# Kernel optimization log

Measured on AMD Instinct MI355X. Metric: run time of the kernel, lower is better.

Reference implementation:

```python
import jax, jax.numpy as jnp
import numpy as np

N_NODES = 100000


def gcn_conv(x, edge_index, W, b, n_nodes):
    """PyG GCNConv: add self-loops, symmetric deg norm, linear, scatter-add, bias."""
    self_loops = jnp.arange(n_nodes, dtype=edge_index.dtype)
    src = jnp.concatenate([edge_index[0], self_loops])  # [E+N]
    dst = jnp.concatenate([edge_index[1], self_loops])  # [E+N]
    xw = x @ W  # [N, out]
    deg = jax.ops.segment_sum(jnp.ones_like(dst, dtype=xw.dtype), dst, num_segments=n_nodes)
    deg_inv_sqrt = jnp.where(deg > 0, jax.lax.rsqrt(deg), 0.0)
    norm = deg_inv_sqrt[src] * deg_inv_sqrt[dst]  # [E+N]
    msg = xw[src] * norm[:, None]                 # [E+N, out]
    out = jax.ops.segment_sum(msg, dst, num_segments=n_nodes)
    return out + b


def setup_inputs() -> dict:
    key = jax.random.key(0)
    ks = jax.random.split(key, 8)
    n, e, d_in, h = N_NODES, 3200000, 128, 16
    x = jax.random.normal(ks[0], (n, d_in), dtype=jnp.float32)
    edge_index = jax.random.randint(ks[1], (2, e), 0, n, dtype=jnp.int64)
    W1 = jax.random.normal(ks[2], (d_in, h), dtype=jnp.float32) / np.sqrt(d_in)
    b1 = jnp.zeros((h,), dtype=jnp.float32)
    W2 = jax.random.normal(ks[3], (h, h), dtype=jnp.float32) / np.sqrt(h)
    b2 = jnp.zeros((h,), dtype=jnp.float32)
    W_lin = jax.random.normal(ks[4], (h, 1), dtype=jnp.float32) / np.sqrt(h)
    b_lin = jnp.zeros((1,), dtype=jnp.float32)
    return {"x": x, "edge_index": edge_index, "W1": W1, "b1": b1,
            "W2": W2, "b2": b2, "W_lin": W_lin, "b_lin": b_lin}


def reference(x, edge_index, W1, b1, W2, b2, W_lin, b_lin):
    n = x.shape[0]
    h = gcn_conv(x, edge_index, W1, b1, n)
    h = jax.nn.relu(h)
    # dropout is identity in eval mode (training=False)
    h = gcn_conv(h, edge_index, W2, b2, n)
    h = jax.nn.relu(h)
    out = h @ W_lin + b_lin  # [N, 1]
    return out.squeeze(-1)   # [N]
```

## Files before the change

kernel.cpp:

```cpp
#include <hip/hip_runtime.h>
#include <hip/hip_fp16.h>

#define DIN 128
#define HDIM 16
#define NB 512
#define BDIV_MAX 256
#define CAPB 7168
#define HSTR 17
#define BIN_EPT 16
#define BINSZ (256 * BIN_EPT)
#define FXS 65536.0f
#define FXI (1.0f / 65536.0f)

__device__ __forceinline__ float4 f4add(float4 a, float4 b) {
    return make_float4(a.x + b.x, a.y + b.y, a.z + b.z, a.w + b.w);
}

__device__ __forceinline__ float4 h4_to_f4(uint2 u) {
    __half2 a = *(__half2*)&u.x, b = *(__half2*)&u.y;
    float2 fa = __half22float2(a), fb = __half22float2(b);
    return make_float4(fa.x, fa.y, fb.x, fb.y);
}
__device__ __forceinline__ uint2 f4_to_h4(float4 v) {
    __half2 a = __floats2half2_rn(v.x, v.y);
    __half2 b = __floats2half2_rn(v.z, v.w);
    uint2 u;
    u.x = *(unsigned*)&a;
    u.y = *(unsigned*)&b;
    return u;
}

__device__ __forceinline__ int load_idx(const void* ei, long long i, int is64) {
    return is64 ? (int)((const long long*)ei)[i] : ((const int*)ei)[i];
}

__device__ __forceinline__ void fx_acc(int* a, float4 v) {
    atomicAdd(a + 0, __float2int_rn(v.x * FXS));
    atomicAdd(a + 1, __float2int_rn(v.y * FXS));
    atomicAdd(a + 2, __float2int_rn(v.z * FXS));
    atomicAdd(a + 3, __float2int_rn(v.w * FXS));
}

__global__ __launch_bounds__(256) void k_main(const void* __restrict__ ei, long long E,
                                              int bdiv, unsigned Mdiv,
                                              int* __restrict__ bcur,
                                              unsigned int* __restrict__ recs,
                                              const float* __restrict__ x,
                                              const float* __restrict__ W1,
                                              unsigned int* __restrict__ y1,
                                              int n, int nbin) {
    __shared__ int cnt[NB];
    __shared__ int base[NB];
    __shared__ float Ws[DIN * HDIM];
    int tid = threadIdx.x;
    if ((int)blockIdx.x < nbin) {
        unsigned probe = ((const unsigned*)ei)[1 + 2 * (tid & 63)];
        int is64 = (__ballot(probe != 0) == 0ull) ? 1 : 0;
        cnt[tid] = 0; cnt[tid + 256] = 0;
        __syncthreads();
        long long e0 = (long long)blockIdx.x * BINSZ;
        int s[BIN_EPT], dl[BIN_EPT], b[BIN_EPT];
        if (e0 + BINSZ <= E) {
            int d[BIN_EPT];
            if (is64) {
                const longlong2* ps = (const longlong2*)((const long long*)ei + e0);
                const longlong2* pd = (const longlong2*)((const long long*)ei + E + e0);
#pragma unroll
                for (int i = 0; i < BIN_EPT / 2; i++) {
                    longlong2 vs = ps[i * 256 + tid];
                    longlong2 vd = pd[i * 256 + tid];
                    s[2 * i + 0] = (int)vs.x; s[2 * i + 1] = (int)vs.y;
                    d[2 * i + 0] = (int)vd.x; d[2 * i + 1] = (int)vd.y;
                }
            } else {
                const int4* ps = (const int4*)((const int*)ei + e0);
                const int4* pd = (const int4*)((const int*)ei + E + e0);
#pragma unroll
                for (int i = 0; i < BIN_EPT / 4; i++) {
                    int4 vs = ps[i * 256 + tid];
                    int4 vd = pd[i * 256 + tid];
                    s[4 * i + 0] = vs.x; s[4 * i + 1] = vs.y;
                    s[4 * i + 2] = vs.z; s[4 * i + 3] = vs.w;
                    d[4 * i + 0] = vd.x; d[4 * i + 1] = vd.y;
                    d[4 * i + 2] = vd.z; d[4 * i + 3] = vd.w;
                }
            }
#pragma unroll
            for (int i = 0; i < BIN_EPT; i++) {
                int bb = Mdiv ? (int)__umulhi((unsigned)d[i], Mdiv) : d[i];
                b[i] = bb;
                dl[i] = d[i] - bb * bdiv;
                atomicAdd(&cnt[bb], 1);
            }
        } else {
#pragma unroll
            for (int i = 0; i < BIN_EPT; i++) {
                long long e = e0 + (long long)i * 256 + tid;
                if (e < E) {
                    s[i] = load_idx(ei, e, is64);
                    int d = load_idx(ei, E + e, is64);
                    int bb = Mdiv ? (int)__umulhi((unsigned)d, Mdiv) : d;
                    b[i] = bb;
                    dl[i] = d - bb * bdiv;
                    atomicAdd(&cnt[bb], 1);
                } else {
                    b[i] = -1;
                }
            }
        }
        __syncthreads();
        {
            int t = tid;
            base[t] = atomicAdd(&bcur[t], cnt[t]); cnt[t] = 0;
            t = tid + 256;
            base[t] = atomicAdd(&bcur[t], cnt[t]); cnt[t] = 0;
        }
        __syncthreads();
#pragma unroll
        for (int i = 0; i < BIN_EPT; i++) {
            if (b[i] >= 0) {
                int off = atomicAdd(&cnt[b[i]], 1);
                int pos = base[b[i]] + off;
                if (pos < CAPB) {
                    recs[(size_t)b[i] * CAPB + pos] =
                        ((unsigned)dl[i] << 18) | (unsigned)s[i];
                }
            }
        }
    } else {
        for (int i = tid; i < DIN * HDIM; i += 256) Ws[i] = W1[i];
        __syncthreads();
        int node = ((int)blockIdx.x - nbin) * 256 + tid;
        if (node >= n) return;
        uint2* yr = (uint2*)(y1 + (size_t)node * 8);
        float acc[HDIM];
#pragma unroll
        for (int f = 0; f < HDIM; f++) acc[f] = 0.f;
        const float4* xr = (const float4*)(x + (size_t)node * DIN);
#pragma unroll 8
        for (int k4 = 0; k4 < DIN / 4; k4++) {
            float4 xv = xr[k4];
            int k = k4 * 4;
#pragma unroll
            for (int f = 0; f < HDIM; f++) {
                acc[f] += xv.x * Ws[(k + 0) * HDIM + f];
                acc[f] += xv.y * Ws[(k + 1) * HDIM + f];
                acc[f] += xv.z * Ws[(k + 2) * HDIM + f];
                acc[f] += xv.w * Ws[(k + 3) * HDIM + f];
            }
        }
#pragma unroll
        for (int q = 0; q < 4; q++)
            yr[q] = f4_to_h4(make_float4(acc[q * 4 + 0], acc[q * 4 + 1],
                                         acc[q * 4 + 2], acc[q * 4 + 3]));
    }
}

__global__ __launch_bounds__(512) void k_deg(const unsigned int* __restrict__ recs,
                                             const int* __restrict__ bcur,
                                             float* __restrict__ dis,
                                             unsigned int* __restrict__ y1,
                                             int n, int bdiv) {
    __shared__ int cnt[BDIV_MAX];
    int tid = threadIdx.x, b = blockIdx.x;
    if (tid < BDIV_MAX) cnt[tid] = 0;
    __syncthreads();
    int lo = b * bdiv; if (lo > n) lo = n;
    int hi = lo + bdiv; if (hi > n) hi = n;
    int nd = hi - lo;
    int m = bcur[b]; if (m > CAPB) m = CAPB;
    const unsigned int* r = recs + (size_t)b * CAPB;
    for (int i = tid; i < m; i += 512)
        atomicAdd(&cnt[r[i] >> 18], 1);
    __syncthreads();
    int q = tid & 3, g = tid >> 2;
    uint2* yv = (uint2*)y1;
    for (int j = g; j < nd; j += 128) {
        int node = lo + j;
        float dv = rsqrtf((float)cnt[j] + 1.0f);
        if (q == 0) dis[node] = dv;
        float4 t = h4_to_f4(yv[(size_t)node * 4 + q]);
        yv[(size_t)node * 4 + q] =
            f4_to_h4(make_float4(t.x * dv, t.y * dv, t.z * dv, t.w * dv));
    }
}

__global__ __launch_bounds__(512) void k_agg1(const unsigned int* __restrict__ recs,
                                              const int* __restrict__ bcur,
                                              const float* __restrict__ dis,
                                              const unsigned int* __restrict__ y1,
                                              const float* __restrict__ b1,
                                              const float* __restrict__ W2,
                                              unsigned int* __restrict__ y2,
                                              int n, int bdiv) {
    __shared__ int acc[BDIV_MAX * HSTR];
    __shared__ float4 Ws4[HDIM][4];
    int tid = threadIdx.x, b = blockIdx.x;
    if (tid < HDIM * 4)
        ((float4*)Ws4)[tid] = ((const float4*)W2)[tid];
    int lo = b * bdiv; if (lo > n) lo = n;
    int hi = lo + bdiv; if (hi > n) hi = n;
    int nd = hi - lo;
    for (int i = tid; i < bdiv * HSTR; i += 512) acc[i] = 0;
    __syncthreads();
    int m = bcur[b]; if (m > CAPB) m = CAPB;
    const unsigned int* r = recs + (size_t)b * CAPB;
    const uint2* yv = (const uint2*)y1;
    int q = tid & 3, g = tid >> 2;
    int i = g;
    for (; i + 128 < m; i += 256) {
        unsigned r0 = r[i], r1 = r[i + 128];
        float4 v0 = h4_to_f4(yv[(size_t)(r0 & 0x3FFFFu) * 4 + q]);
        float4 v1 = h4_to_f4(yv[(size_t)(r1 & 0x3FFFFu) * 4 + q]);
        fx_acc(&acc[(r0 >> 18) * HSTR + q * 4], v0);
        fx_acc(&acc[(r1 >> 18) * HSTR + q * 4], v1);
    }
    if (i < m) {
        unsigned r0 = r[i];
        float4 v0 = h4_to_f4(yv[(size_t)(r0 & 0x3FFFFu) * 4 + q]);
        fx_acc(&acc[(r0 >> 18) * HSTR + q * 4], v0);
    }
    __syncthreads();
    float4 bb = ((const float4*)b1)[q];
    for (int j = g; j < nd; j += 128) {
        int node = lo + j;
        float dv = dis[node];
        int* ap = &acc[j * HSTR + q * 4];
        float4 a = make_float4((float)ap[0] * FXI, (float)ap[1] * FXI,
                               (float)ap[2] * FXI, (float)ap[3] * FXI);
        a = f4add(a, h4_to_f4(yv[(size_t)node * 4 + q]));
        float4 h;
        h.x = fmaxf(dv * a.x + bb.x, 0.f);
        h.y = fmaxf(dv * a.y + bb.y, 0.f);
        h.z = fmaxf(dv * a.z + bb.z, 0.f);
        h.w = fmaxf(dv * a.w + bb.w, 0.f);
        float4 o = make_float4(0.f, 0.f, 0.f, 0.f);
#pragma unroll
        for (int k = 0; k < 4; k++) {
            float4 hk;
            hk.x = __shfl(h.x, k, 4); hk.y = __shfl(h.y, k, 4);
            hk.z = __shfl(h.z, k, 4); hk.w = __shfl(h.w, k, 4);
            float hv[4] = {hk.x, hk.y, hk.z, hk.w};
#pragma unroll
            for (int c = 0; c < 4; c++) {
                float4 w = Ws4[k * 4 + c][q];
                o.x += hv[c] * w.x; o.y += hv[c] * w.y;
                o.z += hv[c] * w.z; o.w += hv[c] * w.w;
            }
        }
        ((uint2*)y2)[(size_t)node * 4 + q] =
            f4_to_h4(make_float4(o.x * dv, o.y * dv, o.z * dv, o.w * dv));
    }
}

__global__ __launch_bounds__(512) void k_agg2(const unsigned int* __restrict__ recs,
                                              const int* __restrict__ bcur,
                                              const float* __restrict__ dis,
                                              const unsigned int* __restrict__ y2,
                                              const float* __restrict__ b2,
                                              const float* __restrict__ Wlin,
                                              const float* __restrict__ blin,
                                              float* __restrict__ out,
                                              int n, int bdiv) {
    __shared__ int acc[BDIV_MAX * HSTR];
    int tid = threadIdx.x, b = blockIdx.x;
    int lo = b * bdiv; if (lo > n) lo = n;
    int hi = lo + bdiv; if (hi > n) hi = n;
    int nd = hi - lo;
    for (int i = tid; i < bdiv * HSTR; i += 512) acc[i] = 0;
    __syncthreads();
    int m = bcur[b]; if (m > CAPB) m = CAPB;
    const unsigned int* r = recs + (size_t)b * CAPB;
    const uint2* yv = (const uint2*)y2;
    int q = tid & 3, g = tid >> 2;
    int i = g;
    for (; i + 128 < m; i += 256) {
        unsigned r0 = r[i], r1 = r[i + 128];
        float4 v0 = h4_to_f4(yv[(size_t)(r0 & 0x3FFFFu) * 4 + q]);
        float4 v1 = h4_to_f4(yv[(size_t)(r1 & 0x3FFFFu) * 4 + q]);
        fx_acc(&acc[(r0 >> 18) * HSTR + q * 4], v0);
        fx_acc(&acc[(r1 >> 18) * HSTR + q * 4], v1);
    }
    if (i < m) {
        unsigned r0 = r[i];
        float4 v0 = h4_to_f4(yv[(size_t)(r0 & 0x3FFFFu) * 4 + q]);
        fx_acc(&acc[(r0 >> 18) * HSTR + q * 4], v0);
    }
    __syncthreads();
    float4 bb = ((const float4*)b2)[q];
    float4 wl = ((const float4*)Wlin)[q];
    for (int j = g; j < nd; j += 128) {
        int node = lo + j;
        float dv = dis[node];
        int* ap = &acc[j * HSTR + q * 4];
        float4 a = make_float4((float)ap[0] * FXI, (float)ap[1] * FXI,
                               (float)ap[2] * FXI, (float)ap[3] * FXI);
        a = f4add(a, h4_to_f4(yv[(size_t)node * 4 + q]));
        float v = 0.f;
        v += fmaxf(dv * a.x + bb.x, 0.f) * wl.x;
        v += fmaxf(dv * a.y + bb.y, 0.f) * wl.y;
        v += fmaxf(dv * a.z + bb.z, 0.f) * wl.z;
        v += fmaxf(dv * a.w + bb.w, 0.f) * wl.w;
        v += __shfl_xor(v, 1, 4);
        v += __shfl_xor(v, 2, 4);
        if (q == 0) out[node] = v + blin[0];
    }
}

extern "C" void kernel_launch(void* const* d_in, const int* in_sizes, int n_in,
                              void* d_out, int out_size, void* d_ws, size_t ws_size,
                              hipStream_t stream) {
    const float* x    = (const float*)d_in[0];
    const void*  ei   = d_in[1];
    const float* W1   = (const float*)d_in[2];
    const float* b1   = (const float*)d_in[3];
    const float* W2   = (const float*)d_in[4];
    const float* b2   = (const float*)d_in[5];
    const float* Wlin = (const float*)d_in[6];
    const float* blin = (const float*)d_in[7];
    float* out = (float*)d_out;

    const int n = in_sizes[0] / DIN;
    const long long E = in_sizes[1] / 2;
    const int bdiv = (n + NB - 1) / NB;
    const unsigned Mdiv = (bdiv > 1)
        ? (unsigned)(((1ull << 32) + (unsigned)bdiv - 1) / (unsigned)bdiv) : 0u;

    char* ws = (char*)d_ws;
    size_t off = 0;
    auto alloc = [&](size_t bytes) { char* p = ws + off; off += (bytes + 255) & ~(size_t)255; return p; };
    int*   bcur = (int*)alloc(NB * 4);
    float* dis  = (float*)alloc((size_t)n * 4);
    unsigned int* y1 = (unsigned int*)alloc((size_t)n * 8 * 4);
    unsigned int* y2 = (unsigned int*)alloc((size_t)n * 8 * 4);
    unsigned int* recs = (unsigned int*)alloc((size_t)NB * CAPB * 4);

    const int nb_xw  = (n + 255) / 256;
    const int nb_bin = (int)((E + BINSZ - 1) / BINSZ);

    hipMemsetAsync(bcur, 0, NB * sizeof(int), stream);
    k_main<<<nb_bin + nb_xw, 256, 0, stream>>>(ei, E, bdiv, Mdiv, bcur, recs, x, W1, y1, n, nb_bin);
    k_deg<<<NB, 512, 0, stream>>>(recs, bcur, dis, y1, n, bdiv);
    k_agg1<<<NB, 512, 0, stream>>>(recs, bcur, dis, y1, b1, W2, y2, n, bdiv);
    k_agg2<<<NB, 512, 0, stream>>>(recs, bcur, dis, y2, b2, Wlin, blin, out, n, bdiv);
}
```

Measured before the change: 203.4 us.

## Count degrees with global atomics during binning and stage records in LDS

The binning kernel now runs 512 threads per block and counts in-degrees directly with global atomics on a zeroed per-node array. This replaces the separate degree kernel, which re-read all the binned records, with a simple per-node normalisation kernel. The aggregation kernels copy each bucket's records into shared memory with vector loads and unroll the gather loop four-way to get more loads in flight. The cost is 3.2M scattered global atomics on the degree array and about 28KB of extra LDS per aggregation block, which can lower occupancy.

Result: slower. 294.5 us (+44.8%).

```diff
diff --git a/kernel.cpp b/kernel.cpp
--- a/kernel.cpp
+++ b/kernel.cpp
@@ -8,7 +8,8 @@
 #define CAPB 7168
 #define HSTR 17
 #define BIN_EPT 16
-#define BINSZ (256 * BIN_EPT)
+#define TPB 512
+#define BINSZ (TPB * BIN_EPT)
 #define FXS 65536.0f
 #define FXI (1.0f / 65536.0f)
 
@@ -41,9 +42,10 @@
     atomicAdd(a + 3, __float2int_rn(v.w * FXS));
 }
 
-__global__ __launch_bounds__(256) void k_main(const void* __restrict__ ei, long long E,
+__global__ __launch_bounds__(512) void k_main(const void* __restrict__ ei, long long E,
                                               int bdiv, unsigned Mdiv,
                                               int* __restrict__ bcur,
+                                              int* __restrict__ deg,
                                               unsigned int* __restrict__ recs,
                                               const float* __restrict__ x,
                                               const float* __restrict__ W1,
@@ -56,7 +58,7 @@
     if ((int)blockIdx.x < nbin) {
         unsigned probe = ((const unsigned*)ei)[1 + 2 * (tid & 63)];
         int is64 = (__ballot(probe != 0) == 0ull) ? 1 : 0;
-        cnt[tid] = 0; cnt[tid + 256] = 0;
+        cnt[tid] = 0;
         __syncthreads();
         long long e0 = (long long)blockIdx.x * BINSZ;
         int s[BIN_EPT], dl[BIN_EPT], b[BIN_EPT];
@@ -67,8 +69,8 @@
                 const longlong2* pd = (const longlong2*)((const long long*)ei + E + e0);
 #pragma unroll
                 for (int i = 0; i < BIN_EPT / 2; i++) {
-                    longlong2 vs = ps[i * 256 + tid];
-                    longlong2 vd = pd[i * 256 + tid];
+                    longlong2 vs = ps[i * TPB + tid];
+                    longlong2 vd = pd[i * TPB + tid];
                     s[2 * i + 0] = (int)vs.x; s[2 * i + 1] = (int)vs.y;
                     d[2 * i + 0] = (int)vd.x; d[2 * i + 1] = (int)vd.y;
                 }
@@ -77,8 +79,8 @@
                 const int4* pd = (const int4*)((const int*)ei + E + e0);
 #pragma unroll
                 for (int i = 0; i < BIN_EPT / 4; i++) {
-                    int4 vs = ps[i * 256 + tid];
-                    int4 vd = pd[i * 256 + tid];
+                    int4 vs = ps[i * TPB + tid];
+                    int4 vd = pd[i * TPB + tid];
                     s[4 * i + 0] = vs.x; s[4 * i + 1] = vs.y;
                     s[4 * i + 2] = vs.z; s[4 * i + 3] = vs.w;
                     d[4 * i + 0] = vd.x; d[4 * i + 1] = vd.y;
@@ -91,11 +93,12 @@
                 b[i] = bb;
                 dl[i] = d[i] - bb * bdiv;
                 atomicAdd(&cnt[bb], 1);
+                atomicAdd(&deg[d[i]], 1);
             }
         } else {
 #pragma unroll
             for (int i = 0; i < BIN_EPT; i++) {
-                long long e = e0 + (long long)i * 256 + tid;
+                long long e = e0 + (long long)i * TPB + tid;
                 if (e < E) {
                     s[i] = load_idx(ei, e, is64);
                     int d = load_idx(ei, E + e, is64);
@@ -103,18 +106,15 @@
                     b[i] = bb;
                     dl[i] = d - bb * bdiv;
                     atomicAdd(&cnt[bb], 1);
+                    atomicAdd(&deg[d], 1);
                 } else {
                     b[i] = -1;
                 }
             }
         }
         __syncthreads();
-        {
-            int t = tid;
-            base[t] = atomicAdd(&bcur[t], cnt[t]); cnt[t] = 0;
-            t = tid + 256;
-            base[t] = atomicAdd(&bcur[t], cnt[t]); cnt[t] = 0;
-        }
+        base[tid] = atomicAdd(&bcur[tid], cnt[tid]);
+        cnt[tid] = 0;
         __syncthreads();
 #pragma unroll
         for (int i = 0; i < BIN_EPT; i++) {
@@ -128,9 +128,9 @@
             }
         }
     } else {
-        for (int i = tid; i < DIN * HDIM; i += 256) Ws[i] = W1[i];
+        for (int i = tid; i < DIN * HDIM; i += TPB) Ws[i] = W1[i];
         __syncthreads();
-        int node = ((int)blockIdx.x - nbin) * 256 + tid;
+        int node = ((int)blockIdx.x - nbin) * TPB + tid;
         if (node >= n) return;
         uint2* yr = (uint2*)(y1 + (size_t)node * 8);
         float acc[HDIM];
@@ -156,33 +156,24 @@
     }
 }
 
-__global__ __launch_bounds__(512) void k_deg(const unsigned int* __restrict__ recs,
-                                             const int* __restrict__ bcur,
+__global__ __launch_bounds__(512) void k_mid(const int* __restrict__ deg,
                                              float* __restrict__ dis,
-                                             unsigned int* __restrict__ y1,
-                                             int n, int bdiv) {
-    __shared__ int cnt[BDIV_MAX];
-    int tid = threadIdx.x, b = blockIdx.x;
-    if (tid < BDIV_MAX) cnt[tid] = 0;
-    __syncthreads();
-    int lo = b * bdiv; if (lo > n) lo = n;
-    int hi = lo + bdiv; if (hi > n) hi = n;
-    int nd = hi - lo;
-    int m = bcur[b]; if (m > CAPB) m = CAPB;
-    const unsigned int* r = recs + (size_t)b * CAPB;
-    for (int i = tid; i < m; i += 512)
-        atomicAdd(&cnt[r[i] >> 18], 1);
-    __syncthreads();
-    int q = tid & 3, g = tid >> 2;
-    uint2* yv = (uint2*)y1;
-    for (int j = g; j < nd; j += 128) {
-        int node = lo + j;
-        float dv = rsqrtf((float)cnt[j] + 1.0f);
-        if (q == 0) dis[node] = dv;
-        float4 t = h4_to_f4(yv[(size_t)node * 4 + q]);
-        yv[(size_t)node * 4 + q] =
-            f4_to_h4(make_float4(t.x * dv, t.y * dv, t.z * dv, t.w * dv));
-    }
+                                             unsigned int* __restrict__ y1, int n) {
+    int node = blockIdx.x * 512 + threadIdx.x;
+    if (node >= n) return;
+    float dv = rsqrtf((float)deg[node] + 1.0f);
+    dis[node] = dv;
+    uint4* yr = (uint4*)(y1 + (size_t)node * 8);
+    uint4 u0 = yr[0], u1 = yr[1];
+    auto sc = [&](unsigned u) -> unsigned {
+        __half2 h = *(__half2*)&u;
+        float2 f = __half22float2(h);
+        __half2 r = __floats2half2_rn(f.x * dv, f.y * dv);
+        return *(unsigned*)&r;
+    };
+    u0.x = sc(u0.x); u0.y = sc(u0.y); u0.z = sc(u0.z); u0.w = sc(u0.w);
+    u1.x = sc(u1.x); u1.y = sc(u1.y); u1.z = sc(u1.z); u1.w = sc(u1.w);
+    yr[0] = u0; yr[1] = u1;
 }
 
 __global__ __launch_bounds__(512) void k_agg1(const unsigned int* __restrict__ recs,
@@ -194,6 +185,7 @@
                                               unsigned int* __restrict__ y2,
                                               int n, int bdiv) {
     __shared__ int acc[BDIV_MAX * HSTR];
+    __shared__ unsigned int sh[CAPB];
     __shared__ float4 Ws4[HDIM][4];
     int tid = threadIdx.x, b = blockIdx.x;
     if (tid < HDIM * 4)
@@ -202,21 +194,27 @@
     int hi = lo + bdiv; if (hi > n) hi = n;
     int nd = hi - lo;
     for (int i = tid; i < bdiv * HSTR; i += 512) acc[i] = 0;
+    int m = bcur[b]; if (m > CAPB) m = CAPB;
+    const uint4* r4 = (const uint4*)(recs + (size_t)b * CAPB);
+    int m4 = (m + 3) >> 2;
+    for (int k = tid; k < m4; k += 512) ((uint4*)sh)[k] = r4[k];
     __syncthreads();
-    int m = bcur[b]; if (m > CAPB) m = CAPB;
-    const unsigned int* r = recs + (size_t)b * CAPB;
     const uint2* yv = (const uint2*)y1;
     int q = tid & 3, g = tid >> 2;
     int i = g;
-    for (; i + 128 < m; i += 256) {
-        unsigned r0 = r[i], r1 = r[i + 128];
+    for (; i + 384 < m; i += 512) {
+        unsigned r0 = sh[i], r1 = sh[i + 128], r2 = sh[i + 256], r3 = sh[i + 384];
         float4 v0 = h4_to_f4(yv[(size_t)(r0 & 0x3FFFFu) * 4 + q]);
         float4 v1 = h4_to_f4(yv[(size_t)(r1 & 0x3FFFFu) * 4 + q]);
+        float4 v2 = h4_to_f4(yv[(size_t)(r2 & 0x3FFFFu) * 4 + q]);
+        float4 v3 = h4_to_f4(yv[(size_t)(r3 & 0x3FFFFu) * 4 + q]);
         fx_acc(&acc[(r0 >> 18) * HSTR + q * 4], v0);
         fx_acc(&acc[(r1 >> 18) * HSTR + q * 4], v1);
-    }
-    if (i < m) {
-        unsigned r0 = r[i];
+        fx_acc(&acc[(r2 >> 18) * HSTR + q * 4], v2);
+        fx_acc(&acc[(r3 >> 18) * HSTR + q * 4], v3);
+    }
+    for (; i < m; i += 128) {
+        unsigned r0 = sh[i];
         float4 v0 = h4_to_f4(yv[(size_t)(r0 & 0x3FFFFu) * 4 + q]);
         fx_acc(&acc[(r0 >> 18) * HSTR + q * 4], v0);
     }
@@ -263,26 +261,33 @@
                                               float* __restrict__ out,
                                               int n, int bdiv) {
     __shared__ int acc[BDIV_MAX * HSTR];
+    __shared__ unsigned int sh[CAPB];
     int tid = threadIdx.x, b = blockIdx.x;
     int lo = b * bdiv; if (lo > n) lo = n;
     int hi = lo + bdiv; if (hi > n) hi = n;
     int nd = hi - lo;
     for (int i = tid; i < bdiv * HSTR; i += 512) acc[i] = 0;
+    int m = bcur[b]; if (m > CAPB) m = CAPB;
+    const uint4* r4 = (const uint4*)(recs + (size_t)b * CAPB);
+    int m4 = (m + 3) >> 2;
+    for (int k = tid; k < m4; k += 512) ((uint4*)sh)[k] = r4[k];
     __syncthreads();
-    int m = bcur[b]; if (m > CAPB) m = CAPB;
-    const unsigned int* r = recs + (size_t)b * CAPB;
     const uint2* yv = (const uint2*)y2;
     int q = tid & 3, g = tid >> 2;
     int i = g;
-    for (; i + 128 < m; i += 256) {
-        unsigned r0 = r[i], r1 = r[i + 128];
+    for (; i + 384 < m; i += 512) {
+        unsigned r0 = sh[i], r1 = sh[i + 128], r2 = sh[i + 256], r3 = sh[i + 384];
         float4 v0 = h4_to_f4(yv[(size_t)(r0 & 0x3FFFFu) * 4 + q]);
         float4 v1 = h4_to_f4(yv[(size_t)(r1 & 0x3FFFFu) * 4 + q]);
+        float4 v2 = h4_to_f4(yv[(size_t)(r2 & 0x3FFFFu) * 4 + q]);
+        float4 v3 = h4_to_f4(yv[(size_t)(r3 & 0x3FFFFu) * 4 + q]);
         fx_acc(&acc[(r0 >> 18) * HSTR + q * 4], v0);
         fx_acc(&acc[(r1 >> 18) * HSTR + q * 4], v1);
-    }
-    if (i < m) {
-        unsigned r0 = r[i];
+        fx_acc(&acc[(r2 >> 18) * HSTR + q * 4], v2);
+        fx_acc(&acc[(r3 >> 18) * HSTR + q * 4], v3);
+    }
+    for (; i < m; i += 128) {
+        unsigned r0 = sh[i];
         float4 v0 = h4_to_f4(yv[(size_t)(r0 & 0x3FFFFu) * 4 + q]);
         fx_acc(&acc[(r0 >> 18) * HSTR + q * 4], v0);
     }
@@ -329,18 +334,21 @@
     char* ws = (char*)d_ws;
     size_t off = 0;
     auto alloc = [&](size_t bytes) { char* p = ws + off; off += (bytes + 255) & ~(size_t)255; return p; };
-    int*   bcur = (int*)alloc(NB * 4);
+    int*   zb   = (int*)alloc((size_t)(NB + n) * 4);
+    int*   bcur = zb;
+    int*   deg  = zb + NB;
     float* dis  = (float*)alloc((size_t)n * 4);
     unsigned int* y1 = (unsigned int*)alloc((size_t)n * 8 * 4);
     unsigned int* y2 = (unsigned int*)alloc((size_t)n * 8 * 4);
     unsigned int* recs = (unsigned int*)alloc((size_t)NB * CAPB * 4);
 
-    const int nb_xw  = (n + 255) / 256;
+    const int nb_xw  = (n + TPB - 1) / TPB;
     const int nb_bin = (int)((E + BINSZ - 1) / BINSZ);
-
-    hipMemsetAsync(bcur, 0, NB * sizeof(int), stream);
-    k_main<<<nb_bin + nb_xw, 256, 0, stream>>>(ei, E, bdiv, Mdiv, bcur, recs, x, W1, y1, n, nb_bin);
-    k_deg<<<NB, 512, 0, stream>>>(recs, bcur, dis, y1, n, bdiv);
+    const int nb_mid = (n + 511) / 512;
+
+    hipMemsetAsync(zb, 0, (size_t)(NB + n) * sizeof(int), stream);
+    k_main<<<nb_bin + nb_xw, TPB, 0, stream>>>(ei, E, bdiv, Mdiv, bcur, deg, recs, x, W1, y1, n, nb_bin);
+    k_mid<<<nb_mid, 512, 0, stream>>>(deg, dis, y1, n);
     k_agg1<<<NB, 512, 0, stream>>>(recs, bcur, dis, y1, b1, W2, y2, n, bdiv);
     k_agg2<<<NB, 512, 0, stream>>>(recs, bcur, dis, y2, b2, Wlin, blin, out, n, bdiv);
 }
```
